# Optimization experiments

Measured on AMD Instinct MI355X. Metric: run time of the kernel, lower is better.

Reference implementation:

```python
import jax, jax.numpy as jnp
import numpy as np

B, C1, C2, N1, N2 = 8, 16, 32, 256, 128


def _masks():
    # static numpy masks, mirroring EquivariantLayer.__init__
    n_max, n_min = max(N1, N2), min(N1, N2)
    k = np.arange(n_max)
    k[k > n_max // 2] -= n_max
    mask = np.abs(k) <= n_min / 2            # |k| <= n_min/2 (both nyquists)
    mask2 = mask[: n_max // 2 + 1].copy()    # taken BEFORE removing neg nyquist
    nyq_pos = k == n_min / 2
    nyq_pos2 = nyq_pos[: n_max // 2 + 1]
    nyq_neg = k == -n_min / 2
    mask[nyq_neg] = False                    # drop negative nyquist row
    return mask, mask2, nyq_pos, nyq_pos2

MASK, MASK2, NYQ_POS, NYQ_POS2 = _masks()


def rot90_kernel(t):
    # 90-deg rotation about grid point [0,0] for periodic kernels:
    # transpose last two dims, keep column 0, reverse remaining columns
    t = jnp.swapaxes(t, -1, -2)
    return jnp.concatenate([t[..., :1], t[..., 1:][..., ::-1]], axis=-1)


def symmetric_kernel(kernel):
    # average over the 8 elements of D4 (rotations + transpose*rotations)
    k1 = kernel
    k2 = rot90_kernel(k1)
    k3 = rot90_kernel(k2)
    k4 = rot90_kernel(k3)
    k5 = jnp.swapaxes(k1, -1, -2)
    k6 = rot90_kernel(k5)
    k7 = rot90_kernel(k6)
    k8 = rot90_kernel(k7)
    return (k1 + k2 + k3 + k4 + k5 + k6 + k7 + k8) / 8.0


def _forward(f, kernel):
    F = jnp.fft.rfft2(f)                                  # [b,c1,N1,N1//2+1]
    # downsample: zero nyquist modes, truncate spectrum, rescale
    F = jnp.where(jnp.asarray(NYQ_POS)[None, None, :, None], 0, F)
    F = jnp.where(jnp.asarray(NYQ_POS2)[None, None, None, :], 0, F)
    F = F[:, :, MASK, :][:, :, :, MASK2] * (N2 / N1) ** 2  # [b,c1,N2,N2//2+1]
    # spectral convolution with D4-symmetrized kernel
    K = jnp.fft.rfft2(symmetric_kernel(kernel))            # [1,c1,c2,N2,N2//2+1]
    conv = jnp.einsum('bcnk,cdnk->bdnk', F, K[0])          # sum over input channels
    return jnp.fft.irfft2(F), jnp.fft.irfft2(conv)


def setup_inputs() -> dict:
    key = jax.random.key(0)
    kf, kk = jax.random.split(key)
    f = jax.random.normal(kf, (B, C1, N1, N1), dtype=jnp.float32)
    eps = 0.1
    kernel = eps * (2.0 * jax.random.uniform(kk, (1, C1, C2, N2, N2), dtype=jnp.float32) - 1.0)
    return {"f": f, "kernel": kernel}


def reference(f, kernel):
    return _forward(f, kernel)
```

## Files before the change

### kernel.cpp

```cpp
#include <hip/hip_runtime.h>

#define PI_F 3.14159265358979f

__device__ __forceinline__ float2 cmul(float2 a, float2 b) {
    return make_float2(a.x * b.x - a.y * b.y, a.x * b.y + a.y * b.x);
}
__device__ __forceinline__ float2 cadd(float2 a, float2 b) { return make_float2(a.x + b.x, a.y + b.y); }
__device__ __forceinline__ float2 csub(float2 a, float2 b) { return make_float2(a.x - b.x, a.y - b.y); }
__device__ __forceinline__ float2 shflx(float2 v, int m) {
    return make_float2(__shfl_xor(v.x, m, 64), __shfl_xor(v.y, m, 64));
}
__device__ __forceinline__ float2 shfli(float2 v, int src) {
    return make_float2(__shfl(v.x, src, 64), __shfl(v.y, src, 64));
}
__device__ __forceinline__ int brev6(int x) { return (int)(__brev((unsigned)x) >> 26); }

template<bool INV>
__device__ __forceinline__ void tw_init(int lane, float2* w, float* sg) {
#pragma unroll
    for (int t = 0; t < 6; ++t) {
        int m = 32 >> t;
        bool up = (lane & m) != 0;
        int pos = lane & (m - 1);
        float ang = (INV ? PI_F : -PI_F) * (float)pos / (float)m;
        float sn, cs;
        __sincosf(ang, &sn, &cs);
        w[t]  = up ? make_float2(cs, sn) : make_float2(1.f, 0.f);
        sg[t] = up ? -1.f : 1.f;
    }
}

__device__ __forceinline__ float2 fft64s(float2 v, const float2* w, const float* sg) {
#pragma unroll
    for (int t = 0; t < 6; ++t) {
        int m = 32 >> t;
        float2 p = shflx(v, m);
        float2 d = make_float2(fmaf(sg[t], v.x, p.x), fmaf(sg[t], v.y, p.y));
        v = cmul(d, w[t]);
    }
    return v;
}

__global__ __launch_bounds__(512) void kfft(const float* __restrict__ kin,
                                            float* __restrict__ kout) {
    __shared__ float2 X[128 * 65];
    int img = blockIdx.x;
    int lane = threadIdx.x & 63, wv = threadIdx.x >> 6;
    float2 w[6]; float sg[6];
    tw_init<false>(lane, w, sg);
    float sn, cs;
    __sincosf(-PI_F * (float)lane * (1.0f / 64.0f), &sn, &cs);
    float2 w64 = make_float2(cs, sn);
    const float2* in2 = (const float2*)(kin + (size_t)img * 16384);
    int b6 = brev6(lane);
    int gm = (64 - lane) & 63;
#pragma unroll 2
    for (int rr = 0; rr < 16; ++rr) {
        int r = wv * 16 + rr;
        float2 z = in2[r * 64 + lane];
        z = fft64s(z, w, sg);
        z = shfli(z, b6);
        float2 zm = shfli(z, gm);
        float ar = z.x + zm.x, ai = z.y - zm.y;
        float br = z.x - zm.x, bi = z.y + zm.y;
        float p = w64.x * br - w64.y * bi, q = w64.x * bi + w64.y * br;
        X[r * 65 + lane] = make_float2(0.5f * (ar + q), 0.5f * (ai - p));
    }
    __syncthreads();
    float2 c0[8], c1[8];
#pragma unroll
    for (int cc = 0; cc < 8; ++cc) {
        int k = wv * 8 + cc;
        c0[cc] = X[lane * 65 + k];
        c1[cc] = X[(lane + 64) * 65 + k];
    }
    __syncthreads();
    float* Rr = (float*)X;
#pragma unroll
    for (int cc = 0; cc < 8; ++cc) {
        int k = wv * 8 + cc;
        float2 r0 = c0[cc], r1 = c1[cc];
        float2 t = r0;
        r0 = cadd(t, r1);
        r1 = cmul(csub(t, r1), w64);
        r0 = fft64s(r0, w, sg);
        r1 = fft64s(r1, w, sg);
        Rr[(2 * b6) * 65 + k]     = r0.x;
        Rr[(2 * b6 + 1) * 65 + k] = r1.x;
    }
    __syncthreads();
    float* ko = kout + (size_t)img * 8192;
    for (int i = threadIdx.x; i < 8192; i += 512) {
        int n = i >> 6, k = i & 63;
        float t1 = Rr[n * 65 + k];
        float t2 = Rr[((128 - n) & 127) * 65 + k];
        float t3, t4;
        if (n < 64) {
            t3 = Rr[k * 65 + n];
            t4 = Rr[((128 - k) & 127) * 65 + n];
        } else {
            int c = 128 - n; if (c > 63) c = 63;
            t3 = Rr[((128 - k) & 127) * 65 + c];
            t4 = Rr[k * 65 + c];
        }
        ko[i] = 0.25f * (t1 + t2 + t3 + t4);
    }
}

__global__ __launch_bounds__(256) void rfft256(const float* __restrict__ f,
                                               float2* __restrict__ G) {
    int lane = threadIdx.x & 63, wv = threadIdx.x >> 6;
    int row = blockIdx.x * 4 + wv;
    float2 w[6]; float sg[6];
    tw_init<false>(lane, w, sg);
    float sn, cs;
    __sincosf(-PI_F * (float)lane * (1.0f / 64.0f), &sn, &cs);
    float2 w64 = make_float2(cs, sn);
    __sincosf(-PI_F * (float)lane * (1.0f / 128.0f), &sn, &cs);
    float2 wu = make_float2(cs, sn);
    const float2* x = (const float2*)(f + (size_t)row * 256);
    float2 r0 = x[lane], r1 = x[lane + 64];
    float2 t = r0;
    r0 = cadd(t, r1);
    r1 = cmul(csub(t, r1), w64);
    r0 = fft64s(r0, w, sg);
    r1 = fft64s(r1, w, sg);
    int srcK = brev6(lane >> 1);
    int srcM = brev6((64 - ((lane + 1) >> 1)) & 63);
    float2 e0 = shfli(r0, srcK), o0 = shfli(r1, srcK);
    float2 zk = (lane & 1) ? o0 : e0;
    float2 e1 = shfli(r0, srcM), o1 = shfli(r1, srcM);
    float2 zm = (lane & 1) ? o1 : e1;
    float ar = zk.x + zm.x, ai = zk.y - zm.y;
    float br = zk.x - zm.x, bi = zk.y + zm.y;
    float p = wu.x * br - wu.y * bi, q = wu.x * bi + wu.y * br;
    G[(size_t)row * 64 + lane] = make_float2(0.5f * (ar + q), 0.5f * (ai - p));
}

__global__ __launch_bounds__(512) void fcol256(const float2* __restrict__ G,
                                               float2* __restrict__ FH) {
    __shared__ float2 S[256 * 33];
    int img = blockIdx.x >> 1, h = blockIdx.x & 1;
    int lane = threadIdx.x & 63, wv = threadIdx.x >> 6;
    float2 w[6]; float sg[6];
    tw_init<false>(lane, w, sg);
    float sn, cs;
    __sincosf(-PI_F * (float)lane * (1.0f / 64.0f), &sn, &cs);
    float2 w64 = make_float2(cs, sn);
    __sincosf(-PI_F * (float)lane * (1.0f / 128.0f), &sn, &cs);
    float2 w128a = make_float2(cs, sn);
    __sincosf(-PI_F * (float)(lane + 64) * (1.0f / 128.0f), &sn, &cs);
    float2 w128b = make_float2(cs, sn);
    const float2* src = G + (size_t)img * 16384 + h * 32;
    for (int i = threadIdx.x; i < 8192; i += 512) {
        int r = i >> 5, c = i & 31;
        S[r * 33 + c] = src[(size_t)r * 64 + c];
    }
    __syncthreads();
    float2 q0[4], q1[4], q2[4], q3[4];
#pragma unroll
    for (int cc = 0; cc < 4; ++cc) {
        int c = wv * 4 + cc;
        q0[cc] = S[(lane)       * 33 + c];
        q1[cc] = S[(lane +  64) * 33 + c];
        q2[cc] = S[(lane + 128) * 33 + c];
        q3[cc] = S[(lane + 192) * 33 + c];
    }
    __syncthreads();
    int b6 = brev6(lane);
#pragma unroll
    for (int cc = 0; cc < 4; ++cc) {
        int c = wv * 4 + cc;
        float2 r0 = q0[cc], r1 = q1[cc], r2 = q2[cc], r3 = q3[cc], t;
        t = r0; r0 = cadd(t, r2); r2 = cmul(csub(t, r2), w128a);
        t = r1; r1 = cadd(t, r3); r3 = cmul(csub(t, r3), w128b);
        t = r0; r0 = cadd(t, r1); r1 = cmul(csub(t, r1), w64);
        t = r2; r2 = cadd(t, r3); r3 = cmul(csub(t, r3), w64);
        r0 = fft64s(r0, w, sg); r1 = fft64s(r1, w, sg);
        r2 = fft64s(r2, w, sg); r3 = fft64s(r3, w, sg);
        float2 vv[4] = { r0, r2, r1, r3 };
#pragma unroll
        for (int j = 0; j < 4; ++j) {
            int n = 4 * b6 + j;
            int r = (n < 64) ? n : ((n >= 193) ? n - 128 : -1);
            if (r >= 0) S[r * 33 + c] = make_float2(vv[j].x * 0.25f, vv[j].y * 0.25f);
        }
    }
    __syncthreads();
    float2* dst = FH + (size_t)img * 8192 + h * 32;
    for (int i = threadIdx.x; i < 4096; i += 512) {
        int r = i >> 5, c = i & 31;
        float2 v = (r == 64) ? make_float2(0.f, 0.f) : S[r * 33 + c];
        dst[(size_t)r * 64 + c] = v;
    }
}

__global__ __launch_bounds__(256) void einsum_rk(const float2* __restrict__ F,
                                                 const float* __restrict__ K,
                                                 float2* __restrict__ C) {
    __shared__ float2 Ft[128 * 32];
    int nkg = blockIdx.x >> 1, dh = blockIdx.x & 1;
    int nk0 = nkg * 32;
    int t = threadIdx.x;
    for (int i = t; i < 4096; i += 256) {
        int bc = i >> 5, nl = i & 31;
        Ft[i] = F[(size_t)bc * 8192 + nk0 + nl];
    }
    __syncthreads();
    int nl = t & 31;
    int dg = t >> 5;
    int nk = nk0 + nl;
#pragma unroll
    for (int dd = 0; dd < 2; ++dd) {
        int d = dh * 16 + dd * 8 + dg;
        float2 acc[8] = {};
#pragma unroll
        for (int c = 0; c < 16; ++c) {
            float kv = K[(size_t)(c * 32 + d) * 8192 + nk];
#pragma unroll
            for (int b = 0; b < 8; ++b) {
                float2 fv = Ft[(b * 16 + c) * 32 + nl];
                acc[b].x += fv.x * kv;
                acc[b].y += fv.y * kv;
            }
        }
#pragma unroll
        for (int b = 0; b < 8; ++b)
            C[(size_t)(b * 32 + d) * 8192 + nk] = acc[b];
    }
}

__global__ __launch_bounds__(512) void ifuse(const float2* __restrict__ FH,
                                             const float2* __restrict__ CV,
                                             float* __restrict__ out) {
    __shared__ float2 S[128 * 65];
    int img = blockIdx.x;
    int lane = threadIdx.x & 63, wv = threadIdx.x >> 6;
    float2 w[6]; float sg[6];
    tw_init<true>(lane, w, sg);
    float sn, cs;
    __sincosf(PI_F * (float)lane * (1.0f / 64.0f), &sn, &cs);
    float2 w64 = make_float2(cs, sn);
    const float2* src = (img < 128) ? (FH + (size_t)img * 8192)
                                    : (CV + (size_t)(img - 128) * 8192);
    float2* dst = (float2*)(out + (size_t)img * 16384);
    for (int i = threadIdx.x; i < 8192; i += 512) {
        int r = i >> 6, c = i & 63;
        S[r * 65 + c] = src[i];
    }
    __syncthreads();
    float2 c0[8], c1[8];
#pragma unroll
    for (int cc = 0; cc < 8; ++cc) {
        int k = wv * 8 + cc;
        c0[cc] = S[lane * 65 + k];
        c1[cc] = S[(lane + 64) * 65 + k];
    }
    __syncthreads();
    int b6 = brev6(lane);
#pragma unroll
    for (int cc = 0; cc < 8; ++cc) {
        int k = wv * 8 + cc;
        float2 r0 = c0[cc], r1 = c1[cc];
        float2 t = r0;
        r0 = cadd(t, r1);
        r1 = cmul(csub(t, r1), w64);
        r0 = fft64s(r0, w, sg);
        r1 = fft64s(r1, w, sg);
        S[(2 * b6) * 65 + k]     = r0;
        S[(2 * b6 + 1) * 65 + k] = r1;
    }
    __syncthreads();
#pragma unroll 2
    for (int rr = 0; rr < 16; ++rr) {
        int m = wv * 16 + rr;
        float2 X = S[m * 65 + lane];
        float2 Xm = shfli(X, (64 - lane) & 63);
        if (lane == 0) Xm = make_float2(0.f, 0.f);
        float er = 0.5f * (X.x + Xm.x), ei = 0.5f * (X.y - Xm.y);
        float br = 0.5f * (X.x - Xm.x), bi = 0.5f * (X.y + Xm.y);
        float orr = w64.x * br - w64.y * bi, oi = w64.x * bi + w64.y * br;
        float2 Z = make_float2(er - oi, ei + orr);
        Z = fft64s(Z, w, sg);
        Z = shfli(Z, b6);
        dst[m * 64 + lane] = make_float2(Z.x * (1.0f / 8192.0f), Z.y * (1.0f / 8192.0f));
    }
}

extern "C" void kernel_launch(void* const* d_in, const int* in_sizes, int n_in,
                              void* d_out, int out_size, void* d_ws, size_t ws_size,
                              hipStream_t stream) {
    const float* f   = (const float*)d_in[0];
    const float* kin = (const float*)d_in[1];
    float* out = (float*)d_out;
    char* ws = (char*)d_ws;

    float2* G    = (float2*)ws;
    float2* CONV = (float2*)ws;
    float2* FHAT = (float2*)(ws + 16777216);
    float*  Kr   = (float*)(ws + 33554432);

    kfft<<<512, 512, 0, stream>>>(kin, Kr);
    rfft256<<<8192, 256, 0, stream>>>(f, G);
    fcol256<<<256, 512, 0, stream>>>(G, FHAT);
    einsum_rk<<<512, 256, 0, stream>>>(FHAT, Kr, CONV);
    ifuse<<<384, 512, 0, stream>>>(FHAT, CONV, out);
}
```

Before: 188.9 us.

## Batch rows per wave in rfft, widen einsum blocks, vectorize kernel output stores

Four separate tweaks go in together. In kfft, one bit-reversal shuffle is removed by computing the mirrored source lane and twiddle in bit-reversed order and storing at the bit-reversed index. The symmetrized kernel output is written as float4 instead of scalar floats. rfft256 now processes 8 rows per wave with 8x fewer blocks, amortizing twiddle setup. einsum_rk has each block cover all 32 output channels with 512 threads, reusing the loaded F values across two d values and using fma. The cost is fewer blocks, which lowers parallelism in rfft and einsum.

```diff
diff --git a/kernel.cpp b/kernel.cpp
--- a/kernel.cpp
+++ b/kernel.cpp
@@ -48,23 +48,24 @@
     int lane = threadIdx.x & 63, wv = threadIdx.x >> 6;
     float2 w[6]; float sg[6];
     tw_init<false>(lane, w, sg);
+    int b6 = brev6(lane);
     float sn, cs;
     __sincosf(-PI_F * (float)lane * (1.0f / 64.0f), &sn, &cs);
     float2 w64 = make_float2(cs, sn);
+    __sincosf(-PI_F * (float)b6 * (1.0f / 64.0f), &sn, &cs);
+    float2 wub = make_float2(cs, sn);
     const float2* in2 = (const float2*)(kin + (size_t)img * 16384);
-    int b6 = brev6(lane);
-    int gm = (64 - lane) & 63;
+    int gm2 = brev6((64 - b6) & 63);
 #pragma unroll 2
     for (int rr = 0; rr < 16; ++rr) {
         int r = wv * 16 + rr;
         float2 z = in2[r * 64 + lane];
         z = fft64s(z, w, sg);
-        z = shfli(z, b6);
-        float2 zm = shfli(z, gm);
+        float2 zm = shfli(z, gm2);
         float ar = z.x + zm.x, ai = z.y - zm.y;
         float br = z.x - zm.x, bi = z.y + zm.y;
-        float p = w64.x * br - w64.y * bi, q = w64.x * bi + w64.y * br;
-        X[r * 65 + lane] = make_float2(0.5f * (ar + q), 0.5f * (ai - p));
+        float p = wub.x * br - wub.y * bi, q = wub.x * bi + wub.y * br;
+        X[r * 65 + b6] = make_float2(0.5f * (ar + q), 0.5f * (ai - p));
     }
     __syncthreads();
     float2 c0[8], c1[8];
@@ -89,28 +90,35 @@
         Rr[(2 * b6 + 1) * 65 + k] = r1.x;
     }
     __syncthreads();
-    float* ko = kout + (size_t)img * 8192;
-    for (int i = threadIdx.x; i < 8192; i += 512) {
-        int n = i >> 6, k = i & 63;
-        float t1 = Rr[n * 65 + k];
-        float t2 = Rr[((128 - n) & 127) * 65 + k];
-        float t3, t4;
-        if (n < 64) {
-            t3 = Rr[k * 65 + n];
-            t4 = Rr[((128 - k) & 127) * 65 + n];
-        } else {
-            int c = 128 - n; if (c > 63) c = 63;
-            t3 = Rr[((128 - k) & 127) * 65 + c];
-            t4 = Rr[k * 65 + c];
+    float4* ko4 = (float4*)(kout + (size_t)img * 8192);
+    for (int i = threadIdx.x; i < 2048; i += 512) {
+        int n = i >> 4, k4 = (i & 15) << 2;
+        float4 o;
+        float* op = (float*)&o;
+#pragma unroll
+        for (int m = 0; m < 4; ++m) {
+            int k = k4 + m;
+            float t1 = Rr[n * 65 + k];
+            float t2 = Rr[((128 - n) & 127) * 65 + k];
+            float t3, t4;
+            if (n < 64) {
+                t3 = Rr[k * 65 + n];
+                t4 = Rr[((128 - k) & 127) * 65 + n];
+            } else {
+                int c2 = 128 - n; if (c2 > 63) c2 = 63;
+                t3 = Rr[((128 - k) & 127) * 65 + c2];
+                t4 = Rr[k * 65 + c2];
+            }
+            op[m] = 0.25f * (t1 + t2 + t3 + t4);
         }
-        ko[i] = 0.25f * (t1 + t2 + t3 + t4);
+        ko4[i] = o;
     }
 }
 
 __global__ __launch_bounds__(256) void rfft256(const float* __restrict__ f,
                                                float2* __restrict__ G) {
     int lane = threadIdx.x & 63, wv = threadIdx.x >> 6;
-    int row = blockIdx.x * 4 + wv;
+    int row0 = (blockIdx.x * 4 + wv) * 8;
     float2 w[6]; float sg[6];
     tw_init<false>(lane, w, sg);
     float sn, cs;
@@ -118,23 +126,27 @@
     float2 w64 = make_float2(cs, sn);
     __sincosf(-PI_F * (float)lane * (1.0f / 128.0f), &sn, &cs);
     float2 wu = make_float2(cs, sn);
-    const float2* x = (const float2*)(f + (size_t)row * 256);
-    float2 r0 = x[lane], r1 = x[lane + 64];
-    float2 t = r0;
-    r0 = cadd(t, r1);
-    r1 = cmul(csub(t, r1), w64);
-    r0 = fft64s(r0, w, sg);
-    r1 = fft64s(r1, w, sg);
     int srcK = brev6(lane >> 1);
     int srcM = brev6((64 - ((lane + 1) >> 1)) & 63);
-    float2 e0 = shfli(r0, srcK), o0 = shfli(r1, srcK);
-    float2 zk = (lane & 1) ? o0 : e0;
-    float2 e1 = shfli(r0, srcM), o1 = shfli(r1, srcM);
-    float2 zm = (lane & 1) ? o1 : e1;
-    float ar = zk.x + zm.x, ai = zk.y - zm.y;
-    float br = zk.x - zm.x, bi = zk.y + zm.y;
-    float p = wu.x * br - wu.y * bi, q = wu.x * bi + wu.y * br;
-    G[(size_t)row * 64 + lane] = make_float2(0.5f * (ar + q), 0.5f * (ai - p));
+#pragma unroll 2
+    for (int rr = 0; rr < 8; ++rr) {
+        size_t row = (size_t)(row0 + rr);
+        const float2* x = (const float2*)(f + row * 256);
+        float2 r0 = x[lane], r1 = x[lane + 64];
+        float2 t = r0;
+        r0 = cadd(t, r1);
+        r1 = cmul(csub(t, r1), w64);
+        r0 = fft64s(r0, w, sg);
+        r1 = fft64s(r1, w, sg);
+        float2 e0 = shfli(r0, srcK), o0 = shfli(r1, srcK);
+        float2 zk = (lane & 1) ? o0 : e0;
+        float2 e1 = shfli(r0, srcM), o1 = shfli(r1, srcM);
+        float2 zm = (lane & 1) ? o1 : e1;
+        float ar = zk.x + zm.x, ai = zk.y - zm.y;
+        float br = zk.x - zm.x, bi = zk.y + zm.y;
+        float p = wu.x * br - wu.y * bi, q = wu.x * bi + wu.y * br;
+        G[row * 64 + lane] = make_float2(0.5f * (ar + q), 0.5f * (ai - p));
+    }
 }
 
 __global__ __launch_bounds__(512) void fcol256(const float2* __restrict__ G,
@@ -195,38 +207,42 @@
     }
 }
 
-__global__ __launch_bounds__(256) void einsum_rk(const float2* __restrict__ F,
+__global__ __launch_bounds__(512) void einsum_rk(const float2* __restrict__ F,
                                                  const float* __restrict__ K,
                                                  float2* __restrict__ C) {
     __shared__ float2 Ft[128 * 32];
-    int nkg = blockIdx.x >> 1, dh = blockIdx.x & 1;
-    int nk0 = nkg * 32;
+    int nk0 = blockIdx.x * 32;
     int t = threadIdx.x;
-    for (int i = t; i < 4096; i += 256) {
+    for (int i = t; i < 4096; i += 512) {
         int bc = i >> 5, nl = i & 31;
         Ft[i] = F[(size_t)bc * 8192 + nk0 + nl];
     }
     __syncthreads();
-    int nl = t & 31;
-    int dg = t >> 5;
+    int nl = t & 31, dg = t >> 5;
     int nk = nk0 + nl;
-#pragma unroll
-    for (int dd = 0; dd < 2; ++dd) {
-        int d = dh * 16 + dd * 8 + dg;
-        float2 acc[8] = {};
-#pragma unroll
-        for (int c = 0; c < 16; ++c) {
+    float2 acc[2][8] = {};
+#pragma unroll
+    for (int c = 0; c < 16; ++c) {
+        float2 fv[8];
+#pragma unroll
+        for (int b = 0; b < 8; ++b) fv[b] = Ft[(b * 16 + c) * 32 + nl];
+#pragma unroll
+        for (int j = 0; j < 2; ++j) {
+            int d = j * 16 + dg;
             float kv = K[(size_t)(c * 32 + d) * 8192 + nk];
 #pragma unroll
             for (int b = 0; b < 8; ++b) {
-                float2 fv = Ft[(b * 16 + c) * 32 + nl];
-                acc[b].x += fv.x * kv;
-                acc[b].y += fv.y * kv;
+                acc[j][b].x = fmaf(fv[b].x, kv, acc[j][b].x);
+                acc[j][b].y = fmaf(fv[b].y, kv, acc[j][b].y);
             }
         }
+    }
+#pragma unroll
+    for (int j = 0; j < 2; ++j) {
+        int d = j * 16 + dg;
 #pragma unroll
         for (int b = 0; b < 8; ++b)
-            C[(size_t)(b * 32 + d) * 8192 + nk] = acc[b];
+            C[(size_t)(b * 32 + d) * 8192 + nk] = acc[j][b];
     }
 }
 
@@ -301,8 +317,8 @@
     float*  Kr   = (float*)(ws + 33554432);
 
     kfft<<<512, 512, 0, stream>>>(kin, Kr);
-    rfft256<<<8192, 256, 0, stream>>>(f, G);
+    rfft256<<<1024, 256, 0, stream>>>(f, G);
     fcol256<<<256, 512, 0, stream>>>(G, FHAT);
-    einsum_rk<<<512, 256, 0, stream>>>(FHAT, Kr, CONV);
+    einsum_rk<<<256, 512, 0, stream>>>(FHAT, Kr, CONV);
     ifuse<<<384, 512, 0, stream>>>(FHAT, CONV, out);
 }
```

After: 181.7 us. 1.04x faster.
